# Kernel optimization log

Hardware: AMD Instinct MI355X
Metric: run time of the kernel (lower is better)

Reference implementation:

```python
import jax, jax.numpy as jnp
import numpy as np

D_MODEL = 768
NUM_HEADS = 12
HEAD_DIM = D_MODEL // NUM_HEADS
BATCH = 1
SEQ = 4096


def setup_inputs() -> dict:
    key = jax.random.key(0)
    ks = jax.random.split(key, 11)
    s = 0.02
    return {
        "q": jax.random.normal(ks[0], (BATCH, SEQ, D_MODEL), jnp.float32),
        "k": jax.random.normal(ks[1], (BATCH, SEQ, D_MODEL), jnp.float32),
        "v": jax.random.normal(ks[2], (BATCH, SEQ, D_MODEL), jnp.float32),
        "Wq": jax.random.normal(ks[3], (D_MODEL, D_MODEL), jnp.float32) * s,
        "bq": jnp.zeros((D_MODEL,), jnp.float32),
        "Wk": jax.random.normal(ks[4], (D_MODEL, D_MODEL), jnp.float32) * s,
        "bk": jnp.zeros((D_MODEL,), jnp.float32),
        "Wv": jax.random.normal(ks[5], (D_MODEL, D_MODEL), jnp.float32) * s,
        "bv": jnp.zeros((D_MODEL,), jnp.float32),
        "Wo": jax.random.normal(ks[6], (D_MODEL, D_MODEL), jnp.float32) * s,
        "bo": jnp.zeros((D_MODEL,), jnp.float32),
    }


def reference(q, k, v, Wq, bq, Wk, bk, Wv, bv, Wo, bo):
    B, S, D = q.shape
    H, Hd = NUM_HEADS, HEAD_DIM
    # linear projections (torch Linear: x @ W.T + b)
    qh = (q @ Wq.T + bq).reshape(B, S, H, Hd).transpose(0, 2, 1, 3)  # [B,H,S,Hd]
    kh = (k @ Wk.T + bk).reshape(B, S, H, Hd).transpose(0, 2, 1, 3)
    vh = (v @ Wv.T + bv).reshape(B, S, H, Hd).transpose(0, 2, 1, 3)
    scale = 1.0 / jnp.sqrt(jnp.asarray(Hd, qh.dtype))
    scores = jnp.einsum("bhsd,bhtd->bhst", qh, kh) * scale  # [B,H,S,S]
    weights = jax.nn.softmax(scores, axis=-1)
    attn = jnp.einsum("bhst,bhtd->bhsd", weights, vh)  # [B,H,S,Hd]
    attn = attn.transpose(0, 2, 1, 3).reshape(B, S, D)
    return attn @ Wo.T + bo
```

## Files before the change

### kernel.cpp

```cpp
#include <hip/hip_runtime.h>

#define S_LEN 4096
#define DMODEL 768
#define NHEAD 12
#define HD 64

typedef __bf16 bf16x8 __attribute__((ext_vector_type(8)));
typedef float f32x4 __attribute__((ext_vector_type(4)));
typedef float f32x16 __attribute__((ext_vector_type(16)));
typedef unsigned short u16x8 __attribute__((ext_vector_type(8)));
typedef unsigned short u16x4 __attribute__((ext_vector_type(4)));
typedef _Float16 f16x4 __attribute__((ext_vector_type(4)));

#if __has_builtin(__builtin_amdgcn_exp2f)
#define EXP2F(x) __builtin_amdgcn_exp2f(x)
#else
#define EXP2F(x) exp2f(x)
#endif

#define MFMA32(a, b, c) __builtin_amdgcn_mfma_f32_32x32x16_bf16(a, b, c, 0, 0, 0)

__device__ __forceinline__ unsigned short f2bf(float f) {
  unsigned int u = __float_as_uint(f);
  u += 0x7fffu + ((u >> 16) & 1u);
  return (unsigned short)(u >> 16);
}

__device__ __forceinline__ void gload_lds16(const void* g, void* l) {
  __builtin_amdgcn_global_load_lds(
      (__attribute__((address_space(1))) void*)g,
      (__attribute__((address_space(3))) void*)l, 16, 0, 0);
}

struct CvtArgs {
  const float* src[4];
  unsigned short* dst[4];
};

__global__ __launch_bounds__(256) void cvt_kernel(CvtArgs a) {
  const int seg = blockIdx.y;
  const int i = (blockIdx.x * 256 + threadIdx.x) * 8;
  const float* s = a.src[seg] + i;
  u16x8 o;
#pragma unroll
  for (int j = 0; j < 8; ++j) o[j] = f2bf(s[j]);
  *reinterpret_cast<u16x8*>(a.dst[seg] + i) = o;
}

struct QkvArgs {
  const float* A[3];
  const unsigned short* W[3];
  const float* bias[3];
  unsigned short* dst[3];
  float scale[3];
};

__global__ __launch_bounds__(256) void qkv_gemm(QkvArgs a) {
  __shared__ unsigned char lds[32768];
  const int z = blockIdx.z;
  const float* __restrict__ A = a.A[z];
  const unsigned short* __restrict__ B = a.W[z];
  const float* __restrict__ bias = a.bias[z];
  unsigned short* __restrict__ dst = a.dst[z];
  const float scale = a.scale[z];

  const int tid = threadIdx.x;
  const int lane = tid & 63;
  const int w = tid >> 6;
  const int wr = w >> 1, wc = w & 1;
  const int c = lane & 15, g = lane >> 4;
  const int m0 = blockIdx.x * 128;
  const int n0 = blockIdx.y * 128;

  f32x4 acc[4][4] = {};

  for (int kt = 0; kt < DMODEL / 64; ++kt) {
#pragma unroll
    for (int p = 0; p < 4; ++p) {
      const int te = p * 256 + tid;
      const int row = te >> 3;
      const int sb = ((te & 7) * 16) ^ ((row & 7) << 4);
      const float* src = A + (size_t)(m0 + row) * DMODEL + kt * 64 + (sb >> 1);
      const f32x4 lo = *reinterpret_cast<const f32x4*>(src);
      const f32x4 hi = *reinterpret_cast<const f32x4*>(src + 4);
      bf16x8 v;
#pragma unroll
      for (int j = 0; j < 4; ++j) { v[j] = (__bf16)lo[j]; v[4 + j] = (__bf16)hi[j]; }
      *reinterpret_cast<bf16x8*>(&lds[te * 16]) = v;
    }
#pragma unroll
    for (int p = 0; p < 4; ++p) {
      const int te = p * 256 + tid;
      const int row = te >> 3;
      const int sb = ((te & 7) * 16) ^ ((row & 7) << 4);
      gload_lds16(B + (size_t)(n0 + row) * DMODEL + kt * 64 + (sb >> 1),
                  &lds[16384 + te * 16]);
    }
    __syncthreads();

    bf16x8 af[4][2], bfr[4][2];
#pragma unroll
    for (int mb = 0; mb < 4; ++mb)
#pragma unroll
      for (int ks = 0; ks < 2; ++ks) {
        const int row = wr * 64 + mb * 16 + c;
        const int byte = (ks * 64 + g * 16) ^ ((row & 7) << 4);
        af[mb][ks] = *reinterpret_cast<const bf16x8*>(&lds[row * 128 + byte]);
      }
#pragma unroll
    for (int nb = 0; nb < 4; ++nb)
#pragma unroll
      for (int ks = 0; ks < 2; ++ks) {
        const int row = wc * 64 + nb * 16 + c;
        const int byte = (ks * 64 + g * 16) ^ ((row & 7) << 4);
        bfr[nb][ks] = *reinterpret_cast<const bf16x8*>(&lds[16384 + row * 128 + byte]);
      }
    __builtin_amdgcn_s_setprio(1);
#pragma unroll
    for (int ks = 0; ks < 2; ++ks)
#pragma unroll
      for (int mb = 0; mb < 4; ++mb)
#pragma unroll
        for (int nb = 0; nb < 4; ++nb)
          acc[mb][nb] = __builtin_amdgcn_mfma_f32_16x16x32_bf16(
              af[mb][ks], bfr[nb][ks], acc[mb][nb], 0, 0, 0);
    __builtin_amdgcn_s_setprio(0);
    __syncthreads();
  }

#pragma unroll
  for (int mb = 0; mb < 4; ++mb) {
#pragma unroll
    for (int nb = 0; nb < 4; ++nb) {
      const int n = n0 + wc * 64 + nb * 16 + c;
      const float bv = bias[n];
#pragma unroll
      for (int r = 0; r < 4; ++r) {
        const int m = m0 + wr * 64 + mb * 16 + g * 4 + r;
        const float v = (acc[mb][nb][r] + bv) * scale;
        const int hh = n >> 6, hd = n & 63;
        if (z != 2) {
          dst[((size_t)hh * S_LEN + m) * HD + hd] = f2bf(v);
        } else {
          const int mp = (m & ~12) | ((m & 4) << 1) | ((m & 8) >> 1);
          dst[((size_t)hh * HD + hd) * S_LEN + mp] = f2bf(v);
        }
      }
    }
  }
}

__global__ __launch_bounds__(256) void gemm_out(
    const unsigned short* __restrict__ A, const unsigned short* __restrict__ B,
    const float* __restrict__ bias, float* __restrict__ dst) {
  __shared__ unsigned char lds[32768];
  const int tid = threadIdx.x;
  const int lane = tid & 63;
  const int w = tid >> 6;
  const int wr = w >> 1, wc = w & 1;
  const int c = lane & 15, g = lane >> 4;
  const int m0 = blockIdx.x * 128;
  const int n0 = blockIdx.y * 128;

  f32x4 acc[4][4] = {};

  for (int kt = 0; kt < DMODEL / 64; ++kt) {
#pragma unroll
    for (int p = 0; p < 4; ++p) {
      const int te = p * 256 + tid;
      const int row = te >> 3;
      const int sb = ((te & 7) * 16) ^ ((row & 7) << 4);
      gload_lds16(A + (size_t)(m0 + row) * DMODEL + kt * 64 + (sb >> 1), &lds[te * 16]);
      gload_lds16(B + (size_t)(n0 + row) * DMODEL + kt * 64 + (sb >> 1), &lds[16384 + te * 16]);
    }
    __syncthreads();

    bf16x8 af[4][2], bfr[4][2];
#pragma unroll
    for (int mb = 0; mb < 4; ++mb)
#pragma unroll
      for (int ks = 0; ks < 2; ++ks) {
        const int row = wr * 64 + mb * 16 + c;
        const int byte = (ks * 64 + g * 16) ^ ((row & 7) << 4);
        af[mb][ks] = *reinterpret_cast<const bf16x8*>(&lds[row * 128 + byte]);
      }
#pragma unroll
    for (int nb = 0; nb < 4; ++nb)
#pragma unroll
      for (int ks = 0; ks < 2; ++ks) {
        const int row = wc * 64 + nb * 16 + c;
        const int byte = (ks * 64 + g * 16) ^ ((row & 7) << 4);
        bfr[nb][ks] = *reinterpret_cast<const bf16x8*>(&lds[16384 + row * 128 + byte]);
      }
    __builtin_amdgcn_s_setprio(1);
#pragma unroll
    for (int ks = 0; ks < 2; ++ks)
#pragma unroll
      for (int mb = 0; mb < 4; ++mb)
#pragma unroll
        for (int nb = 0; nb < 4; ++nb)
          acc[mb][nb] = __builtin_amdgcn_mfma_f32_16x16x32_bf16(
              af[mb][ks], bfr[nb][ks], acc[mb][nb], 0, 0, 0);
    __builtin_amdgcn_s_setprio(0);
    __syncthreads();
  }

#pragma unroll
  for (int mb = 0; mb < 4; ++mb)
#pragma unroll
    for (int nb = 0; nb < 4; ++nb) {
      const int n = n0 + wc * 64 + nb * 16 + c;
      const float bv = bias[n];
#pragma unroll
      for (int r = 0; r < 4; ++r) {
        const int m = m0 + wr * 64 + mb * 16 + g * 4 + r;
        dst[(size_t)m * DMODEL + n] = acc[mb][nb][r] + bv;
      }
    }
}

__global__ __launch_bounds__(256, 2) void attn_kernel(
    const unsigned short* __restrict__ qh,
    const unsigned short* __restrict__ kh,
    const unsigned short* __restrict__ vtp,
    _Float16* __restrict__ pacc,
    float* __restrict__ prs) {
  __shared__ unsigned char lds[49152];
  const int tid = threadIdx.x;
  const int lane = tid & 63;
  const int w = tid >> 6;
  const int c5 = lane & 31;
  const int h2 = lane >> 5;
  const int hh = blockIdx.y;
  const int split = blockIdx.z;
  const int qw = blockIdx.x * 256 + w * 64;
  const int kv0 = split * (S_LEN / 4);
  const int nkt = (S_LEN / 4) / 64;

  bf16x8 qa0[4], qa1[4];
#pragma unroll
  for (int ks = 0; ks < 4; ++ks) {
    qa0[ks] = *reinterpret_cast<const bf16x8*>(
        qh + ((size_t)hh * S_LEN + qw + c5) * HD + ks * 16 + h2 * 8);
    qa1[ks] = *reinterpret_cast<const bf16x8*>(
        qh + ((size_t)hh * S_LEN + qw + 32 + c5) * HD + ks * 16 + h2 * 8);
  }

  const unsigned short* ksrc =
      kh + ((size_t)hh * S_LEN + kv0 + (tid & 63)) * HD + (tid >> 6) * 8;
  const unsigned short* vsrc =
      vtp + ((size_t)hh * HD + (tid & 63)) * S_LEN + kv0 + (tid >> 6) * 8;
  const int dL = tid * 16;

  auto stage = [&](int bo) {
    gload_lds16(ksrc, &lds[bo + dL]);
    gload_lds16(ksrc + 32, &lds[bo + 4096 + dL]);
    gload_lds16(vsrc, &lds[bo + 8192 + dL]);
    gload_lds16(vsrc + 32, &lds[bo + 12288 + dL]);
    ksrc += 64 * HD;
    vsrc += 64;
  };

  stage(0);
  stage(16384);

  f32x16 accO00 = {}, accO01 = {}, accO10 = {}, accO11 = {};
  float rsA = 0.f, rsB = 0.f;

  auto compute = [&](const unsigned char* Kb, const unsigned char* Vb) {
    f32x16 s0A = {}, s1A = {}, s0B = {}, s1B = {};
    __builtin_amdgcn_s_setprio(1);
#pragma unroll
    for (int ks = 0; ks < 4; ++ks) {
      const unsigned char* kbase = Kb + (ks * 2 + h2) * 1024 + c5 * 16;
      const bf16x8 k0 = *reinterpret_cast<const bf16x8*>(kbase);
      const bf16x8 k1 = *reinterpret_cast<const bf16x8*>(kbase + 512);
      s0A = MFMA32(k0, qa0[ks], s0A);
      s0B = MFMA32(k0, qa1[ks], s0B);
      s1A = MFMA32(k1, qa0[ks], s1A);
      s1B = MFMA32(k1, qa1[ks], s1B);
    }
    __builtin_amdgcn_s_setprio(0);

#pragma unroll
    for (int t = 0; t < 2; ++t)
#pragma unroll
      for (int ss = 0; ss < 2; ++ss) {
        const unsigned char* vbase = Vb + (t * 4 + ss * 2 + h2) * 1024 + c5 * 16;
        const bf16x8 va0 = *reinterpret_cast<const bf16x8*>(vbase);
        const bf16x8 va1 = *reinterpret_cast<const bf16x8*>(vbase + 512);
        bf16x8 pbA, pbB;
        float ra = 0.f, rb = 0.f;
#pragma unroll
        for (int r = 0; r < 8; ++r) {
          const float eA = EXP2F(t ? s1A[ss * 8 + r] : s0A[ss * 8 + r]);
          const float eB = EXP2F(t ? s1B[ss * 8 + r] : s0B[ss * 8 + r]);
          ra += eA; rb += eB;
          pbA[r] = (__bf16)eA;
          pbB[r] = (__bf16)eB;
        }
        rsA += ra; rsB += rb;
        __builtin_amdgcn_s_setprio(1);
        accO00 = MFMA32(va0, pbA, accO00);
        accO01 = MFMA32(va1, pbA, accO01);
        accO10 = MFMA32(va0, pbB, accO10);
        accO11 = MFMA32(va1, pbB, accO11);
        __builtin_amdgcn_s_setprio(0);
      }
  };

  int boC = 0;
  int boS = 32768;
  for (int t = 0; t < nkt; ++t) {
    if (t + 2 < nkt) {
      asm volatile("s_waitcnt vmcnt(4)" ::: "memory");
      __builtin_amdgcn_sched_barrier(0);
      __builtin_amdgcn_s_barrier();
      __builtin_amdgcn_sched_barrier(0);
      stage(boS);
    } else if (t + 1 < nkt) {
      asm volatile("s_waitcnt vmcnt(4)" ::: "memory");
      __builtin_amdgcn_sched_barrier(0);
      __builtin_amdgcn_s_barrier();
      __builtin_amdgcn_sched_barrier(0);
    } else {
      asm volatile("s_waitcnt vmcnt(0)" ::: "memory");
      __builtin_amdgcn_sched_barrier(0);
      __builtin_amdgcn_s_barrier();
      __builtin_amdgcn_sched_barrier(0);
    }
    compute(&lds[boC], &lds[boC + 8192]);
    boC += 16384; if (boC == 49152) boC = 0;
    boS += 16384; if (boS == 49152) boS = 0;
  }

  rsA += __shfl_xor(rsA, 32);
  rsB += __shfl_xor(rsB, 32);
  const size_t hqb0 = ((size_t)split * NHEAD + hh) * S_LEN + qw + c5;
  const size_t hqb1 = hqb0 + 32;
  if (h2 == 0) {
    prs[hqb0] = rsA * 0.015625f;
    prs[hqb1] = rsB * 0.015625f;
  }
#pragma unroll
  for (int dt = 0; dt < 2; ++dt)
#pragma unroll
    for (int rr = 0; rr < 4; ++rr) {
      const int doff = dt * 32 + rr * 8 + h2 * 4;
      f16x4 oA, oB;
#pragma unroll
      for (int j = 0; j < 4; ++j) {
        oA[j] = (_Float16)((dt ? accO01[rr * 4 + j] : accO00[rr * 4 + j]) * 0.015625f);
        oB[j] = (_Float16)((dt ? accO11[rr * 4 + j] : accO10[rr * 4 + j]) * 0.015625f);
      }
      *reinterpret_cast<f16x4*>(pacc + hqb0 * 64 + doff) = oA;
      *reinterpret_cast<f16x4*>(pacc + hqb1 * 64 + doff) = oB;
    }
}

__global__ __launch_bounds__(256) void combine_kernel(
    const _Float16* __restrict__ pacc, const float* __restrict__ prs,
    unsigned short* __restrict__ attb) {
  const int idx = blockIdx.x * 256 + threadIdx.x;
  const int hq = idx >> 4;
  const int d4 = (idx & 15) * 4;
  const int h = hq >> 12;
  const int q = hq & 4095;
  const int HS = NHEAD * S_LEN;
  const size_t o0 = (size_t)hq * 64 + d4;
  float acc4[4] = {0.f, 0.f, 0.f, 0.f};
  float rs = 0.f;
#pragma unroll
  for (int k = 0; k < 4; ++k) {
    const f16x4 av = *reinterpret_cast<const f16x4*>(pacc + o0 + (size_t)k * HS * 64);
#pragma unroll
    for (int j = 0; j < 4; ++j) acc4[j] += (float)av[j];
    rs += prs[hq + k * HS];
  }
  const float inv = 1.f / rs;
  u16x4 ov;
#pragma unroll
  for (int j = 0; j < 4; ++j) ov[j] = f2bf(acc4[j] * inv);
  *reinterpret_cast<u16x4*>(attb + (size_t)q * DMODEL + h * HD + d4) = ov;
}

extern "C" void kernel_launch(void* const* d_in, const int* in_sizes, int n_in,
                              void* d_out, int out_size, void* d_ws, size_t ws_size,
                              hipStream_t stream) {
  (void)in_sizes; (void)n_in; (void)out_size;
  const float* q  = (const float*)d_in[0];
  const float* k  = (const float*)d_in[1];
  const float* v  = (const float*)d_in[2];
  const float* Wq = (const float*)d_in[3];
  const float* bq = (const float*)d_in[4];
  const float* Wk = (const float*)d_in[5];
  const float* bk = (const float*)d_in[6];
  const float* Wv = (const float*)d_in[7];
  const float* bv = (const float*)d_in[8];
  const float* Wo = (const float*)d_in[9];
  const float* bo = (const float*)d_in[10];
  float* out = (float*)d_out;

  const size_t SD = (size_t)S_LEN * DMODEL;
  const size_t DD = (size_t)DMODEL * DMODEL;
  if (ws_size < (7 * SD + 4 * DD) * 2) return;

  unsigned short* ws   = (unsigned short*)d_ws;
  unsigned short* wqb  = ws;
  unsigned short* wkb  = ws + DD;
  unsigned short* wvb  = ws + 2 * DD;
  unsigned short* qhb  = ws + 4 * SD;
  unsigned short* khb  = ws + 5 * SD;
  unsigned short* vtb  = ws + 6 * SD;
  float*          prs  = (float*)(ws + 7 * SD);
  unsigned short* wob  = ws + 7 * SD + 393216;
  _Float16*       pacc = (_Float16*)ws;
  unsigned short* attb = ws + 4 * SD;

  CvtArgs ca;
  ca.src[0] = Wq; ca.dst[0] = wqb;
  ca.src[1] = Wk; ca.dst[1] = wkb;
  ca.src[2] = Wv; ca.dst[2] = wvb;
  ca.src[3] = Wo; ca.dst[3] = wob;
  cvt_kernel<<<dim3(288, 4), 256, 0, stream>>>(ca);

  QkvArgs qa;
  qa.A[0] = q; qa.W[0] = wqb; qa.bias[0] = bq; qa.dst[0] = qhb;
  qa.scale[0] = 0.18033688011112042f;
  qa.A[1] = k; qa.W[1] = wkb; qa.bias[1] = bk; qa.dst[1] = khb;
  qa.scale[1] = 1.0f;
  qa.A[2] = v; qa.W[2] = wvb; qa.bias[2] = bv; qa.dst[2] = vtb;
  qa.scale[2] = 1.0f;
  qkv_gemm<<<dim3(32, 6, 3), 256, 0, stream>>>(qa);

  attn_kernel<<<dim3(S_LEN / 256, NHEAD, 4), 256, 0, stream>>>(
      qhb, khb, vtb, pacc, prs);

  combine_kernel<<<dim3((NHEAD * S_LEN * 16) / 256), 256, 0, stream>>>(
      pacc, prs, attb);

  gemm_out<<<dim3(32, 6), 256, 0, stream>>>(attb, wob, bo, out);
}
```

Measured before the change: 121.4 us.

## Read K/V tiles directly from global memory instead of LDS triple-buffering

Removes the LDS triple-buffered staging of K and V tiles, along with its waitcnt and barrier synchronisation, in the attention kernel. Each wave now loads its K and V MFMA operands straight from global memory, relying on cache hits. This drops LDS traffic and block barriers, but the four waves of a block now each fetch the same K/V data and global load latency is no longer hidden by prefetching.

```diff
diff --git a/kernel.cpp b/kernel.cpp
--- a/kernel.cpp
+++ b/kernel.cpp
@@ -225,7 +225,6 @@
     const unsigned short* __restrict__ vtp,
     _Float16* __restrict__ pacc,
     float* __restrict__ prs) {
-  __shared__ unsigned char lds[49152];
   const int tid = threadIdx.x;
   const int lane = tid & 63;
   const int w = tid >> 6;
@@ -246,55 +245,42 @@
         qh + ((size_t)hh * S_LEN + qw + 32 + c5) * HD + ks * 16 + h2 * 8);
   }
 
-  const unsigned short* ksrc =
-      kh + ((size_t)hh * S_LEN + kv0 + (tid & 63)) * HD + (tid >> 6) * 8;
-  const unsigned short* vsrc =
-      vtp + ((size_t)hh * HD + (tid & 63)) * S_LEN + kv0 + (tid >> 6) * 8;
-  const int dL = tid * 16;
-
-  auto stage = [&](int bo) {
-    gload_lds16(ksrc, &lds[bo + dL]);
-    gload_lds16(ksrc + 32, &lds[bo + 4096 + dL]);
-    gload_lds16(vsrc, &lds[bo + 8192 + dL]);
-    gload_lds16(vsrc + 32, &lds[bo + 12288 + dL]);
-    ksrc += 64 * HD;
-    vsrc += 64;
-  };
-
-  stage(0);
-  stage(16384);
-
   f32x16 accO00 = {}, accO01 = {}, accO10 = {}, accO11 = {};
   float rsA = 0.f, rsB = 0.f;
 
-  auto compute = [&](const unsigned char* Kb, const unsigned char* Vb) {
+  const unsigned short* kb = kh + ((size_t)hh * S_LEN + kv0) * HD;
+  const unsigned short* vb = vtp + (size_t)hh * HD * S_LEN + kv0;
+
+  for (int t = 0; t < nkt; ++t) {
     f32x16 s0A = {}, s1A = {}, s0B = {}, s1B = {};
-    __builtin_amdgcn_s_setprio(1);
 #pragma unroll
     for (int ks = 0; ks < 4; ++ks) {
-      const unsigned char* kbase = Kb + (ks * 2 + h2) * 1024 + c5 * 16;
-      const bf16x8 k0 = *reinterpret_cast<const bf16x8*>(kbase);
-      const bf16x8 k1 = *reinterpret_cast<const bf16x8*>(kbase + 512);
+      const int cc = ks * 2 + h2;
+      const bf16x8 k0 = *reinterpret_cast<const bf16x8*>(kb + (size_t)c5 * HD + cc * 8);
+      const bf16x8 k1 = *reinterpret_cast<const bf16x8*>(kb + (size_t)(32 + c5) * HD + cc * 8);
+      __builtin_amdgcn_s_setprio(1);
       s0A = MFMA32(k0, qa0[ks], s0A);
       s0B = MFMA32(k0, qa1[ks], s0B);
       s1A = MFMA32(k1, qa0[ks], s1A);
       s1B = MFMA32(k1, qa1[ks], s1B);
-    }
-    __builtin_amdgcn_s_setprio(0);
-
-#pragma unroll
-    for (int t = 0; t < 2; ++t)
+      __builtin_amdgcn_s_setprio(0);
+    }
+
+#pragma unroll
+    for (int tq = 0; tq < 2; ++tq)
 #pragma unroll
       for (int ss = 0; ss < 2; ++ss) {
-        const unsigned char* vbase = Vb + (t * 4 + ss * 2 + h2) * 1024 + c5 * 16;
-        const bf16x8 va0 = *reinterpret_cast<const bf16x8*>(vbase);
-        const bf16x8 va1 = *reinterpret_cast<const bf16x8*>(vbase + 512);
+        const int cc = tq * 4 + ss * 2 + h2;
+        const bf16x8 va0 = *reinterpret_cast<const bf16x8*>(
+            vb + (size_t)c5 * S_LEN + cc * 8);
+        const bf16x8 va1 = *reinterpret_cast<const bf16x8*>(
+            vb + (size_t)(32 + c5) * S_LEN + cc * 8);
         bf16x8 pbA, pbB;
         float ra = 0.f, rb = 0.f;
 #pragma unroll
         for (int r = 0; r < 8; ++r) {
-          const float eA = EXP2F(t ? s1A[ss * 8 + r] : s0A[ss * 8 + r]);
-          const float eB = EXP2F(t ? s1B[ss * 8 + r] : s0B[ss * 8 + r]);
+          const float eA = EXP2F(tq ? s1A[ss * 8 + r] : s0A[ss * 8 + r]);
+          const float eB = EXP2F(tq ? s1B[ss * 8 + r] : s0B[ss * 8 + r]);
           ra += eA; rb += eB;
           pbA[r] = (__bf16)eA;
           pbB[r] = (__bf16)eB;
@@ -307,31 +293,9 @@
         accO11 = MFMA32(va1, pbB, accO11);
         __builtin_amdgcn_s_setprio(0);
       }
-  };
-
-  int boC = 0;
-  int boS = 32768;
-  for (int t = 0; t < nkt; ++t) {
-    if (t + 2 < nkt) {
-      asm volatile("s_waitcnt vmcnt(4)" ::: "memory");
-      __builtin_amdgcn_sched_barrier(0);
-      __builtin_amdgcn_s_barrier();
-      __builtin_amdgcn_sched_barrier(0);
-      stage(boS);
-    } else if (t + 1 < nkt) {
-      asm volatile("s_waitcnt vmcnt(4)" ::: "memory");
-      __builtin_amdgcn_sched_barrier(0);
-      __builtin_amdgcn_s_barrier();
-      __builtin_amdgcn_sched_barrier(0);
-    } else {
-      asm volatile("s_waitcnt vmcnt(0)" ::: "memory");
-      __builtin_amdgcn_sched_barrier(0);
-      __builtin_amdgcn_s_barrier();
-      __builtin_amdgcn_sched_barrier(0);
-    }
-    compute(&lds[boC], &lds[boC + 8192]);
-    boC += 16384; if (boC == 49152) boC = 0;
-    boS += 16384; if (boS == 49152) boS = 0;
+
+    kb += 64 * HD;
+    vb += 64;
   }
 
   rsA += __shfl_xor(rsA, 32);
```

Result: slower. 164.1 us (+35.2%).
